# Kernel tuning notes

Hardware: AMD Instinct MI355X
Metric: run time of the kernel (lower is better)

The kernel has to match this reference:

```python
import jax, jax.numpy as jnp
import numpy as np

NUM_CLASSES = 20
K = 3
STRIDE = 32
IMG = 2048


def setup_inputs() -> dict:
    key = jax.random.key(0)
    k1, k2, k3, k4, k5, k6, k7 = jax.random.split(key, 7)
    B, Cin, H, W = 2, 1024, 64, 64
    N = 1000
    feats = jax.random.normal(k1, (B, Cin, H, W), jnp.float32)
    s = 1.0 / np.sqrt(Cin).astype(np.float32)
    w_cls = jax.random.normal(k2, ((NUM_CLASSES + 1) * K * K, Cin), jnp.float32) * s
    b_cls = jax.random.normal(k3, ((NUM_CLASSES + 1) * K * K,), jnp.float32) * 0.01
    w_reg = jax.random.normal(k4, (4 * K * K, Cin), jnp.float32) * s
    b_reg = jax.random.normal(k5, (4 * K * K,), jnp.float32) * 0.01
    # proposals in image pixel coords (x1, y1, x2, y2), guaranteed non-empty
    xy1 = jax.random.randint(k6, (B, N, 2), 0, IMG - 64)
    wh = jax.random.randint(k7, (B, N, 2), STRIDE, 512)
    xy2 = jnp.minimum(xy1 + wh, IMG)
    proposals = jnp.concatenate([xy1, xy2], axis=-1).astype(jnp.int32)
    return {"features": feats, "w_cls": w_cls, "b_cls": b_cls,
            "w_reg": w_reg, "b_reg": b_reg, "proposals": proposals}


def _psroi(scores, proposals, groups):
    """Faithful to the source: adaptive_avg_pool2d bin (0,0) per channel,
    then sum over the K*K channel groups (stride-::K*K indexing in torch)."""
    B, C, H, W = scores.shape
    N = proposals.shape[1]
    p = proposals.astype(jnp.float32) / STRIDE
    x1 = jnp.floor(p[..., 0]).astype(jnp.int32)  # [B,N]
    y1 = jnp.floor(p[..., 1]).astype(jnp.int32)
    x2 = jnp.ceil(p[..., 2]).astype(jnp.int32)
    y2 = jnp.ceil(p[..., 3]).astype(jnp.int32)
    # adaptive_avg_pool2d bin (0,0): rows [0, ceil(h/K)), cols [0, ceil(w/K)) of the crop
    hb = (y2 - y1 + K - 1) // K
    wb = (x2 - x1 + K - 1) // K
    r = jnp.arange(H)
    c = jnp.arange(W)
    rmask = (r[None, None, :] >= y1[..., None]) & (r[None, None, :] < (y1 + hb)[..., None])  # [B,N,H]
    cmask = (c[None, None, :] >= x1[..., None]) & (c[None, None, :] < (x1 + wb)[..., None])  # [B,N,W]
    mask = (rmask[..., :, None] & cmask[..., None, :]).astype(scores.dtype)  # [B,N,H,W]
    denom = (hb * wb).astype(scores.dtype)
    pooled = jnp.einsum('bohw,bnhw->bno', scores, mask) / denom[..., None]  # bin(0,0) avg, all channels
    # channel index = cls_group * K*K + g ; torch ::K*K picks (g, spatial_bin 0) then sums over g
    return pooled.reshape(B, N, groups, K * K).sum(-1)


def reference(features, w_cls, b_cls, w_reg, b_reg, proposals):
    cls_scores = jnp.einsum('bchw,oc->bohw', features, w_cls) + b_cls[None, :, None, None]
    reg_scores = jnp.einsum('bchw,oc->bohw', features, w_reg) + b_reg[None, :, None, None]
    cls_out = _psroi(cls_scores, proposals, NUM_CLASSES + 1)  # [B,N,21]
    reg_out = _psroi(reg_scores, proposals, 4)                # [B,N,4]
    return (cls_out, reg_out)
```

## Files before the change

kernel.cpp:

```cpp
#include <hip/hip_runtime.h>


#define HW 4096
#define NG 25
#define CIN 1024
#define B 2
#define NPROP 1000
#define NCH 2
#define CK (CIN / NCH)
#define NSL 16
#define CS (CK / NSL)
#define MHW (B * NG * HW)

__global__ void rfcn_wfold(const float* __restrict__ w_cls,
                           const float* __restrict__ b_cls,
                           const float* __restrict__ w_reg,
                           const float* __restrict__ b_reg,
                           float* __restrict__ Wred,
                           float* __restrict__ Bred) {
    int i = blockIdx.x * 256 + threadIdx.x;
    if (i < NG * CIN) {
        int g = i >> 10, c = i & (CIN - 1);
        float s = 0.f;
        if (g < 21) {
            #pragma unroll
            for (int k = 0; k < 9; ++k) s += w_cls[(size_t)(g * 9 + k) * CIN + c];
        } else {
            int gr = g - 21;
            #pragma unroll
            for (int k = 0; k < 9; ++k) s += w_reg[(size_t)(gr * 9 + k) * CIN + c];
        }
        Wred[i] = s;
    } else if (i < NG * CIN + NG) {
        int g = i - NG * CIN;
        float s = 0.f;
        if (g < 21) {
            #pragma unroll
            for (int k = 0; k < 9; ++k) s += b_cls[g * 9 + k];
        } else {
            #pragma unroll
            for (int k = 0; k < 9; ++k) s += b_reg[(g - 21) * 9 + k];
        }
        Bred[g] = s;
    }
}

__global__ __launch_bounds__(1024)
void rfcn_proj(const float* __restrict__ feats,
               const float* __restrict__ Wred,
               float* __restrict__ part) {
    const int t = threadIdx.x;
    const int p = t & 63;
    const int sl = __builtin_amdgcn_readfirstlane(t >> 6);
    const int pix0 = blockIdx.x * 64;
    const int chunk = blockIdx.y;
    const int b = blockIdx.z;
    const int c0 = chunk * CK + sl * CS;

    const float* __restrict__ f = feats + ((size_t)b * CIN + c0) * HW + pix0 + p;
    const float* __restrict__ wgt = Wred + c0;

    float acc[NG];
    #pragma unroll
    for (int g = 0; g < NG; ++g) acc[g] = 0.f;

    #pragma unroll
    for (int cc = 0; cc < CS; cc += 16) {
        float fv[16];
        #pragma unroll
        for (int j = 0; j < 16; ++j) fv[j] = f[(size_t)(cc + j) * HW];
        #pragma unroll
        for (int j = 0; j < 16; ++j)
            #pragma unroll
            for (int g = 0; g < NG; ++g)
                acc[g] += fv[j] * wgt[g * CIN + cc + j];
    }

    __shared__ float red[NSL * NG * 64];
    #pragma unroll
    for (int g = 0; g < NG; ++g) red[(sl * NG + g) * 64 + p] = acc[g];
    __syncthreads();

    float* __restrict__ o = part + ((size_t)(chunk * B + b) * NG) * HW + pix0;
    for (int idx = t; idx < NG * 64; idx += 1024) {
        const int g = idx >> 6, pp = idx & 63;
        float s = 0.f;
        #pragma unroll
        for (int ss = 0; ss < NSL; ++ss) s += red[(ss * NG + g) * 64 + pp];
        o[(size_t)g * HW + pp] = s;
    }
}

__global__ __launch_bounds__(1024)
void rfcn_integral_gather(const float* __restrict__ part,
                          const int* __restrict__ props,
                          const float* __restrict__ Bred,
                          float* __restrict__ out) {
    const int m = blockIdx.x;
    const int t = threadIdx.x;
    const int lane = t & 63;
    const int wave = t >> 6;
    const int b = m / NG;
    const int g = m - b * NG;
    __shared__ float tile[64 * 65];

    #pragma unroll
    for (int i = 0; i < 4; ++i) {
        const int idx = i * 1024 + t;
        const float v = part[(size_t)m * HW + idx]
                      + part[(size_t)(B * NG + m) * HW + idx];
        tile[(idx >> 6) * 65 + (idx & 63)] = v;
    }
    __syncthreads();

    #pragma unroll
    for (int i = 0; i < 4; ++i) {
        const int row = wave * 4 + i;
        float v = tile[row * 65 + lane];
        #pragma unroll
        for (int d = 1; d < 64; d <<= 1) {
            float u = __shfl_up(v, (unsigned)d, 64);
            if (lane >= d) v += u;
        }
        tile[row * 65 + lane] = v;
    }
    __syncthreads();

    #pragma unroll
    for (int i = 0; i < 4; ++i) {
        const int col = wave * 4 + i;
        float v = tile[lane * 65 + col];
        #pragma unroll
        for (int d = 1; d < 64; d <<= 1) {
            float u = __shfl_up(v, (unsigned)d, 64);
            if (lane >= d) v += u;
        }
        tile[lane * 65 + col] = v;
    }
    __syncthreads();

    const float bias = Bred[g];
    const int n = t;
    if (n < NPROP) {
        const int4 pr = ((const int4*)props)[b * NPROP + n];
        const int x1 = pr.x >> 5;
        const int y1 = pr.y >> 5;
        const int x2 = (pr.z + 31) >> 5;
        const int y2 = (pr.w + 31) >> 5;
        const int wb = (x2 - x1 + 2) / 3;
        const int hb = (y2 - y1 + 2) / 3;
        const int c2 = x1 + wb - 1;
        const int r2 = y1 + hb - 1;

        float s = tile[r2 * 65 + c2];
        if (x1 > 0)           s -= tile[r2 * 65 + (x1 - 1)];
        if (y1 > 0)           s -= tile[(y1 - 1) * 65 + c2];
        if (x1 > 0 && y1 > 0) s += tile[(y1 - 1) * 65 + (x1 - 1)];
        const float v = bias + s / (float)(hb * wb);
        if (g < 21)
            out[(size_t)(b * NPROP + n) * 21 + g] = v;
        else
            out[(size_t)(B * NPROP * 21) + (size_t)(b * NPROP + n) * 4 + (g - 21)] = v;
    }
}

extern "C" void kernel_launch(void* const* d_in, const int* in_sizes, int n_in,
                              void* d_out, int out_size, void* d_ws, size_t ws_size,
                              hipStream_t stream) {
    const float* feats = (const float*)d_in[0];
    const float* w_cls = (const float*)d_in[1];
    const float* b_cls = (const float*)d_in[2];
    const float* w_reg = (const float*)d_in[3];
    const float* b_reg = (const float*)d_in[4];
    const int*   props = (const int*)d_in[5];
    float* out = (float*)d_out;
    float* ws  = (float*)d_ws;

    float* Wred = ws;
    float* Bred = ws + 25600;
    float* part = ws + 25632;

    rfcn_wfold<<<(NG * CIN + NG + 255) / 256, 256, 0, stream>>>(
        w_cls, b_cls, w_reg, b_reg, Wred, Bred);
    rfcn_proj<<<dim3(HW / 64, NCH, B), 1024, 0, stream>>>(feats, Wred, part);
    rfcn_integral_gather<<<B * NG, 1024, 0, stream>>>(part, props, Bred, out);
}
```

Measured before the change: 27.80 us.

## Process two pixels per thread with float2 loads and rebalance channel split

The projection kernel now has each thread handle two adjacent pixels through float2 loads, so each weight read is reused for twice the work. The channel dimension is split into four chunks instead of two to keep the grid size the same. The shared-memory reduction becomes a two-stage fold that halves the slices before the final sum. The gather kernel now sums four partial buffers with vectorized loads, which adds workspace traffic and raises register pressure from preloading all 16 channels per thread.

```diff
diff --git a/kernel.cpp b/kernel.cpp
--- a/kernel.cpp
+++ b/kernel.cpp
@@ -6,11 +6,12 @@
 #define CIN 1024
 #define B 2
 #define NPROP 1000
-#define NCH 2
+#define NCH 4
 #define CK (CIN / NCH)
 #define NSL 16
 #define CS (CK / NSL)
 #define MHW (B * NG * HW)
+#define PX 128
 
 __global__ void rfcn_wfold(const float* __restrict__ w_cls,
                            const float* __restrict__ b_cls,
@@ -50,44 +51,60 @@
                const float* __restrict__ Wred,
                float* __restrict__ part) {
     const int t = threadIdx.x;
-    const int p = t & 63;
+    const int l = t & 63;
     const int sl = __builtin_amdgcn_readfirstlane(t >> 6);
-    const int pix0 = blockIdx.x * 64;
+    const int pix0 = blockIdx.x * PX;
     const int chunk = blockIdx.y;
     const int b = blockIdx.z;
     const int c0 = chunk * CK + sl * CS;
 
-    const float* __restrict__ f = feats + ((size_t)b * CIN + c0) * HW + pix0 + p;
+    const float2* __restrict__ f2 =
+        (const float2*)feats + (size_t)(b * CIN + c0) * (HW / 2) + (pix0 >> 1) + l;
     const float* __restrict__ wgt = Wred + c0;
 
-    float acc[NG];
-    #pragma unroll
-    for (int g = 0; g < NG; ++g) acc[g] = 0.f;
-
-    #pragma unroll
-    for (int cc = 0; cc < CS; cc += 16) {
-        float fv[16];
-        #pragma unroll
-        for (int j = 0; j < 16; ++j) fv[j] = f[(size_t)(cc + j) * HW];
-        #pragma unroll
-        for (int j = 0; j < 16; ++j)
-            #pragma unroll
-            for (int g = 0; g < NG; ++g)
-                acc[g] += fv[j] * wgt[g * CIN + cc + j];
-    }
-
-    __shared__ float red[NSL * NG * 64];
-    #pragma unroll
-    for (int g = 0; g < NG; ++g) red[(sl * NG + g) * 64 + p] = acc[g];
-    __syncthreads();
-
-    float* __restrict__ o = part + ((size_t)(chunk * B + b) * NG) * HW + pix0;
+    float2 acc[NG];
+    #pragma unroll
+    for (int g = 0; g < NG; ++g) acc[g] = make_float2(0.f, 0.f);
+
+    float2 fv[CS];
+    #pragma unroll
+    for (int j = 0; j < CS; ++j) fv[j] = f2[(size_t)j * (HW / 2)];
+    #pragma unroll
+    for (int j = 0; j < CS; ++j)
+        #pragma unroll
+        for (int g = 0; g < NG; ++g) {
+            const float w = wgt[g * CIN + j];
+            acc[g].x += fv[j].x * w;
+            acc[g].y += fv[j].y * w;
+        }
+
+    __shared__ float2 red2[8 * NG * 64];
+    if (sl >= 8) {
+        #pragma unroll
+        for (int g = 0; g < NG; ++g) red2[((sl - 8) * NG + g) * 64 + l] = acc[g];
+    }
+    __syncthreads();
+    if (sl < 8) {
+        #pragma unroll
+        for (int g = 0; g < NG; ++g) {
+            float2 r = red2[(sl * NG + g) * 64 + l];
+            r.x += acc[g].x; r.y += acc[g].y;
+            red2[(sl * NG + g) * 64 + l] = r;
+        }
+    }
+    __syncthreads();
+
+    float2* __restrict__ o2 =
+        (float2*)part + (size_t)(chunk * B + b) * NG * (HW / 2) + (pix0 >> 1);
     for (int idx = t; idx < NG * 64; idx += 1024) {
-        const int g = idx >> 6, pp = idx & 63;
-        float s = 0.f;
-        #pragma unroll
-        for (int ss = 0; ss < NSL; ++ss) s += red[(ss * NG + g) * 64 + pp];
-        o[(size_t)g * HW + pp] = s;
+        const int g = idx >> 6, l2 = idx & 63;
+        float2 s = make_float2(0.f, 0.f);
+        #pragma unroll
+        for (int ss = 0; ss < 8; ++ss) {
+            const float2 r = red2[(ss * NG + g) * 64 + l2];
+            s.x += r.x; s.y += r.y;
+        }
+        o2[(size_t)g * (HW / 2) + l2] = s;
     }
 }
 
@@ -104,12 +121,21 @@
     const int g = m - b * NG;
     __shared__ float tile[64 * 65];
 
-    #pragma unroll
-    for (int i = 0; i < 4; ++i) {
+    const float2* __restrict__ p2 = (const float2*)part + (size_t)m * (HW / 2);
+    #pragma unroll
+    for (int i = 0; i < 2; ++i) {
         const int idx = i * 1024 + t;
-        const float v = part[(size_t)m * HW + idx]
-                      + part[(size_t)(B * NG + m) * HW + idx];
-        tile[(idx >> 6) * 65 + (idx & 63)] = v;
+        float2 v[NCH];
+        #pragma unroll
+        for (int ch = 0; ch < NCH; ++ch)
+            v[ch] = p2[(size_t)ch * (MHW / 2) + idx];
+        float2 s = make_float2(0.f, 0.f);
+        #pragma unroll
+        for (int ch = 0; ch < NCH; ++ch) { s.x += v[ch].x; s.y += v[ch].y; }
+        const int row = idx >> 5;
+        const int col = (idx & 31) * 2;
+        tile[row * 65 + col]     = s.x;
+        tile[row * 65 + col + 1] = s.y;
     }
     __syncthreads();
 
@@ -182,6 +208,6 @@
 
     rfcn_wfold<<<(NG * CIN + NG + 255) / 256, 256, 0, stream>>>(
         w_cls, b_cls, w_reg, b_reg, Wred, Bred);
-    rfcn_proj<<<dim3(HW / 64, NCH, B), 1024, 0, stream>>>(feats, Wred, part);
+    rfcn_proj<<<dim3(HW / PX, NCH, B), 1024, 0, stream>>>(feats, Wred, part);
     rfcn_integral_gather<<<B * NG, 1024, 0, stream>>>(part, props, Bred, out);
 }
```

New measurement: 28.42 us. 1.02x slower.

## Fuse weight folding into projection kernel and stage folded weights in LDS

Applied to the files above, without the earlier changes.

Removes the separate weight-fold launch. Each projection block now folds its chunk of cls/reg weights (sum over the K*K groups) into shared memory, and the bias fold moves into the gather kernel. The inner loop is restructured to load all CS feature values first, then do per-group dot products using float4 LDS reads. This saves a kernel launch and a global round trip for the folded weights. In exchange, every one of the 256 blocks redundantly re-reads and re-sums 9x the weight slice (about 50KB of LDS plus 115KB of global reads per block), and register pressure rises.

```diff
diff --git a/kernel.cpp b/kernel.cpp
--- a/kernel.cpp
+++ b/kernel.cpp
@@ -12,71 +12,64 @@
 #define CS (CK / NSL)
 #define MHW (B * NG * HW)
 
-__global__ void rfcn_wfold(const float* __restrict__ w_cls,
-                           const float* __restrict__ b_cls,
-                           const float* __restrict__ w_reg,
-                           const float* __restrict__ b_reg,
-                           float* __restrict__ Wred,
-                           float* __restrict__ Bred) {
-    int i = blockIdx.x * 256 + threadIdx.x;
-    if (i < NG * CIN) {
-        int g = i >> 10, c = i & (CIN - 1);
+__global__ __launch_bounds__(1024)
+void rfcn_projf(const float* __restrict__ feats,
+                const float* __restrict__ w_cls,
+                const float* __restrict__ w_reg,
+                float* __restrict__ part) {
+    const int t = threadIdx.x;
+    const int chunk = blockIdx.y;
+    const int b = blockIdx.z;
+    __shared__ float wlds[NG * CK];
+    __shared__ float red[NSL * NG * 64];
+
+    for (int idx = t; idx < NG * CK; idx += 1024) {
+        const int g = idx / CK;
+        const int c = idx - g * CK;
+        const int gc = chunk * CK + c;
         float s = 0.f;
         if (g < 21) {
             #pragma unroll
-            for (int k = 0; k < 9; ++k) s += w_cls[(size_t)(g * 9 + k) * CIN + c];
+            for (int k = 0; k < 9; ++k) s += w_cls[(size_t)(g * 9 + k) * CIN + gc];
         } else {
-            int gr = g - 21;
+            const int gr = g - 21;
             #pragma unroll
-            for (int k = 0; k < 9; ++k) s += w_reg[(size_t)(gr * 9 + k) * CIN + c];
+            for (int k = 0; k < 9; ++k) s += w_reg[(size_t)(gr * 9 + k) * CIN + gc];
         }
-        Wred[i] = s;
-    } else if (i < NG * CIN + NG) {
-        int g = i - NG * CIN;
-        float s = 0.f;
-        if (g < 21) {
-            #pragma unroll
-            for (int k = 0; k < 9; ++k) s += b_cls[g * 9 + k];
-        } else {
-            #pragma unroll
-            for (int k = 0; k < 9; ++k) s += b_reg[(g - 21) * 9 + k];
-        }
-        Bred[g] = s;
+        wlds[idx] = s;
     }
-}
+    __syncthreads();
 
-__global__ __launch_bounds__(1024)
-void rfcn_proj(const float* __restrict__ feats,
-               const float* __restrict__ Wred,
-               float* __restrict__ part) {
-    const int t = threadIdx.x;
     const int p = t & 63;
     const int sl = __builtin_amdgcn_readfirstlane(t >> 6);
     const int pix0 = blockIdx.x * 64;
-    const int chunk = blockIdx.y;
-    const int b = blockIdx.z;
     const int c0 = chunk * CK + sl * CS;
 
     const float* __restrict__ f = feats + ((size_t)b * CIN + c0) * HW + pix0 + p;
-    const float* __restrict__ wgt = Wred + c0;
+    const float4* __restrict__ w4 = (const float4*)(wlds + sl * CS);
 
     float acc[NG];
     #pragma unroll
     for (int g = 0; g < NG; ++g) acc[g] = 0.f;
 
+    float fv[CS];
     #pragma unroll
-    for (int cc = 0; cc < CS; cc += 16) {
-        float fv[16];
+    for (int j = 0; j < CS; ++j) fv[j] = f[(size_t)j * HW];
+
+    #pragma unroll
+    for (int g = 0; g < NG; ++g) {
+        float a = 0.f;
         #pragma unroll
-        for (int j = 0; j < 16; ++j) fv[j] = f[(size_t)(cc + j) * HW];
-        #pragma unroll
-        for (int j = 0; j < 16; ++j)
-            #pragma unroll
-            for (int g = 0; g < NG; ++g)
-                acc[g] += fv[j] * wgt[g * CIN + cc + j];
+        for (int q = 0; q < CS / 4; ++q) {
+            const float4 w = w4[(size_t)g * (CK / 4) + q];
+            a += fv[4 * q]     * w.x;
+            a += fv[4 * q + 1] * w.y;
+            a += fv[4 * q + 2] * w.z;
+            a += fv[4 * q + 3] * w.w;
+        }
+        acc[g] = a;
     }
 
-    __shared__ float red[NSL * NG * 64];
     #pragma unroll
     for (int g = 0; g < NG; ++g) red[(sl * NG + g) * 64 + p] = acc[g];
     __syncthreads();
@@ -92,10 +85,11 @@
 }
 
 __global__ __launch_bounds__(1024)
-void rfcn_integral_gather(const float* __restrict__ part,
-                          const int* __restrict__ props,
-                          const float* __restrict__ Bred,
-                          float* __restrict__ out) {
+void rfcn_ig(const float* __restrict__ part,
+             const int* __restrict__ props,
+             const float* __restrict__ b_cls,
+             const float* __restrict__ b_reg,
+             float* __restrict__ out) {
     const int m = blockIdx.x;
     const int t = threadIdx.x;
     const int lane = t & 63;
@@ -103,6 +97,15 @@
     const int b = m / NG;
     const int g = m - b * NG;
     __shared__ float tile[64 * 65];
+
+    float bias = 0.f;
+    if (g < 21) {
+        #pragma unroll
+        for (int k = 0; k < 9; ++k) bias += b_cls[g * 9 + k];
+    } else {
+        #pragma unroll
+        for (int k = 0; k < 9; ++k) bias += b_reg[(g - 21) * 9 + k];
+    }
 
     #pragma unroll
     for (int i = 0; i < 4; ++i) {
@@ -139,7 +142,6 @@
     }
     __syncthreads();
 
-    const float bias = Bred[g];
     const int n = t;
     if (n < NPROP) {
         const int4 pr = ((const int4*)props)[b * NPROP + n];
@@ -176,12 +178,9 @@
     float* out = (float*)d_out;
     float* ws  = (float*)d_ws;
 
-    float* Wred = ws;
-    float* Bred = ws + 25600;
-    float* part = ws + 25632;
+    float* part = ws;
 
-    rfcn_wfold<<<(NG * CIN + NG + 255) / 256, 256, 0, stream>>>(
-        w_cls, b_cls, w_reg, b_reg, Wred, Bred);
-    rfcn_proj<<<dim3(HW / 64, NCH, B), 1024, 0, stream>>>(feats, Wred, part);
-    rfcn_integral_gather<<<B * NG, 1024, 0, stream>>>(part, props, Bred, out);
+    rfcn_projf<<<dim3(HW / 64, NCH, B), 1024, 0, stream>>>(
+        feats, w_cls, w_reg, part);
+    rfcn_ig<<<B * NG, 1024, 0, stream>>>(part, props, b_cls, b_reg, out);
 }
```

Measured after the change: 31.06 us. 11.7% more time.
